# Kernel optimization log

Hardware: AMD Instinct MI355X
Metric: run time of the kernel (lower is better)

## Reference

```python
import jax, jax.numpy as jnp
import numpy as np


def _leaky(x):
    return jax.nn.leaky_relu(x, 0.01)


def _seq_query(sess_embed, query, batch_idx, B, W1, b1, W2, b2, a, ab):
    # attention weight per node, then segment-sum per session (vectorized torch.split loop)
    q = query[batch_idx]                                   # [T,D]
    w = jax.nn.sigmoid(q @ W1 + b1 + sess_embed @ W2 + b2) @ a + ab  # [T,1]
    return jax.ops.segment_sum(w * sess_embed, batch_idx, num_segments=B)


def setup_inputs() -> dict:
    key = jax.random.key(0)
    ks = jax.random.split(key, 24)
    N, D, B, L, E, G = 50000, 64, 512, 64, 1650000, 2
    T = B * L
    s = 1.0 / float(np.sqrt(D))
    rn = lambda k, sh: jax.random.normal(k, sh, dtype=jnp.float32) * s
    inp = {
        'sess_idx': jax.random.randint(ks[0], (T,), 0, N),
        'edges': jax.random.randint(ks[1], (2, T), 0, T),
        'batch_idx': jnp.repeat(jnp.arange(B, dtype=jnp.int32), L),
        'tar_poi': jax.random.randint(ks[2], (B,), 0, N),
        'y': (jax.random.uniform(ks[3], (B,)) > 0.5).astype(jnp.float32),
        'edge_index': jax.random.randint(ks[4], (2, E), 0, N),
        'dist_vec': jax.random.uniform(ks[5], (E,), dtype=jnp.float32),
        'poi_embed': rn(ks[6], (N, D)),
        'geo_W0': rn(ks[7], (G, D, D)),
        'geo_W1': rn(ks[8], (G, D, D)),
        'ggc_W': rn(ks[9], (D, D)),
        'gru_wih': rn(ks[10], (3 * D, D)),
        'gru_whh': rn(ks[11], (3 * D, D)),
        'gru_bih': jnp.zeros((3 * D,), jnp.float32),
        'gru_bhh': jnp.zeros((3 * D,), jnp.float32),
        'geoq_W1': rn(ks[12], (D, D)), 'geoq_b1': jnp.zeros((D,), jnp.float32),
        'geoq_W2': rn(ks[13], (D, D)), 'geoq_b2': jnp.zeros((D,), jnp.float32),
        'geoq_a': rn(ks[14], (D, 1)), 'geoq_ab': jnp.zeros((1,), jnp.float32),
        'sessq_W1': rn(ks[15], (D, D)), 'sessq_b1': jnp.zeros((D,), jnp.float32),
        'sessq_W2': rn(ks[16], (D, D)), 'sessq_b2': jnp.zeros((D,), jnp.float32),
        'sessq_a': rn(ks[17], (D, 1)), 'sessq_ab': jnp.zeros((1,), jnp.float32),
        'geo_proj': rn(ks[18], (D, D)),
        'sess_proj': rn(ks[19], (D, D)),
        'mlp_W1': rn(ks[20], (4 * D, D)), 'mlp_b1': jnp.zeros((D,), jnp.float32),
        'mlp_W2': rn(ks[21], (D, 1)), 'mlp_b2': jnp.zeros((1,), jnp.float32),
    }
    return inp


def reference(sess_idx, edges, batch_idx, tar_poi, y, edge_index, dist_vec,
              poi_embed, geo_W0, geo_W1, ggc_W, gru_wih, gru_whh, gru_bih, gru_bhh,
              geoq_W1, geoq_b1, geoq_W2, geoq_b2, geoq_a, geoq_ab,
              sessq_W1, sessq_b1, sessq_W2, sessq_b2, sessq_a, sessq_ab,
              geo_proj, sess_proj, mlp_W1, mlp_b1, mlp_W2, mlp_b2):
    N, D = poi_embed.shape
    B = tar_poi.shape[0]
    T = sess_idx.shape[0]
    row, col = edge_index[0], edge_index[1]

    # symmetric degree norm as in Geo_GCN (degree of col)
    deg = jax.ops.segment_sum(jnp.ones_like(dist_vec), col, num_segments=N)
    dinv = jnp.where(deg > 0, deg ** -0.5, 0.0)
    norm = dinv[row] * dinv[col]
    # NOTE: original applies exp(-d**2) twice (once in CTR.forward, once in Geo_GCN)
    dw = jnp.exp(-jnp.exp(-dist_vec ** 2) ** 2)
    val = (dw * norm)[:, None]                              # [E,1]

    geo_feat = poi_embed
    for i in range(geo_W0.shape[0]):
        side = jax.ops.segment_sum(val * geo_feat[col], row, num_segments=N)  # sparse mm
        geo_feat = _leaky(side @ geo_W0[i] + (geo_feat * side) @ geo_W1[i])
        geo_feat = geo_feat / jnp.maximum(
            jnp.linalg.norm(geo_feat, axis=-1, keepdims=True), 1e-12)

    geo_enc = _seq_query(geo_feat[sess_idx], geo_feat[tar_poi], batch_idx, B,
                         geoq_W1, geoq_b1, geoq_W2, geoq_b2, geoq_a, geoq_ab)
    geo_enc_p = geo_enc @ geo_proj

    # Neigh_pooling: mean aggregation at target node
    neigh = jax.ops.segment_sum(poi_embed[row], col, num_segments=N) \
        / jnp.maximum(deg, 1.0)[:, None]
    counts = jax.ops.segment_sum(jnp.ones((T,), poi_embed.dtype), batch_idx,
                                 num_segments=B)[:, None]
    geo_pool = (jax.ops.segment_sum(neigh[sess_idx], batch_idx, num_segments=B)
                / counts) @ geo_proj

    # GatedGraphConv, num_layers=1: sum-aggregate (h W), then GRU cell
    h = poi_embed[sess_idx]
    m = jax.ops.segment_sum((h @ ggc_W)[edges[0]], edges[1], num_segments=T)
    gi = m @ gru_wih.T + gru_bih
    gh = h @ gru_whh.T + gru_bhh
    ir, iz, i_n = jnp.split(gi, 3, axis=-1)
    hr, hz, h_n = jnp.split(gh, 3, axis=-1)
    r = jax.nn.sigmoid(ir + hr)
    z = jax.nn.sigmoid(iz + hz)
    n = jnp.tanh(i_n + r * h_n)
    sess_hidden = _leaky((1.0 - z) * n + z * h)

    sess_enc = _seq_query(sess_hidden, poi_embed[tar_poi], batch_idx, B,
                          sessq_W1, sessq_b1, sessq_W2, sessq_b2, sessq_a, sessq_ab)
    sess_enc_p = sess_enc @ sess_proj
    sess_pool = (jax.ops.segment_sum(poi_embed[sess_idx], batch_idx,
                                     num_segments=B) / counts) @ sess_proj

    bpr = lambda x, pos, neg: jax.nn.softplus((x * neg).sum(-1) - (x * pos).sum(-1))
    con_loss = bpr(geo_enc, geo_pool, sess_pool) + bpr(sess_enc, sess_pool, geo_pool)

    tar_embed = poi_embed[tar_poi]
    tar_geo_embed = geo_feat[tar_poi]
    feats = jnp.concatenate([tar_embed, tar_geo_embed, sess_enc_p, geo_enc_p], axis=-1)
    logits = (_leaky(feats @ mlp_W1 + mlp_b1) @ mlp_W2 + mlp_b2)[:, 0]
    return logits, con_loss, y, tar_embed, tar_geo_embed, geo_enc_p, sess_enc_p
```

## Files before the change

### kernel.cpp

```cpp
#include <hip/hip_runtime.h>
#include <math.h>

#define CDIV(a,b) (((a)+(b)-1)/(b))

__device__ __forceinline__ float wred(float v){
  #pragma unroll
  for (int o = 32; o; o >>= 1) v += __shfl_xor(v, o, 64);
  return v;
}
__device__ __forceinline__ float leakyf(float x){ return x > 0.f ? x : 0.01f * x; }
__device__ __forceinline__ float sigmf(float x){ return 1.f / (1.f + expf(-x)); }
__device__ __forceinline__ float softplusf(float x){
  return fmaxf(x, 0.f) + log1pf(expf(-fabsf(x)));
}

__global__ void k_deg2(const int* __restrict__ row, const int* __restrict__ col,
                       int* __restrict__ deg_row, int* __restrict__ deg_col,
                       int* __restrict__ rank_r, int* __restrict__ rank_c, int E){
  int e = blockIdx.x * blockDim.x + threadIdx.x;
  if (e < E){
    rank_r[e] = atomicAdd(&deg_row[row[e]], 1);
    rank_c[e] = atomicAdd(&deg_col[col[e]], 1);
  }
}

__global__ __launch_bounds__(1024) void k_scan2(const int* __restrict__ in0, int* __restrict__ out0,
                        const int* __restrict__ in1, int* __restrict__ out1,
                        float* __restrict__ dinv, int n){
  __shared__ int wincl[16];
  const int* in  = blockIdx.x ? in1 : in0;
  int* out       = blockIdx.x ? out1 : out0;
  int tid = threadIdx.x, lane = tid & 63, wv = tid >> 6;
  int carry = 0;
  for (int base = 0; base < n; base += 1024){
    int i = base + tid;
    int x = (i < n) ? in[i] : 0;
    int v = x;
    #pragma unroll
    for (int ofs = 1; ofs < 64; ofs <<= 1){
      int t = __shfl_up(v, ofs, 64);
      if (lane >= ofs) v += t;
    }
    if (lane == 63) wincl[wv] = v;
    __syncthreads();
    if (wv == 0 && lane < 16){
      int s = wincl[lane];
      #pragma unroll
      for (int ofs = 1; ofs < 16; ofs <<= 1){
        int t = __shfl_up(s, ofs, 64);
        if (lane >= ofs) s += t;
      }
      wincl[lane] = s;
    }
    __syncthreads();
    int woff = wv ? wincl[wv - 1] : 0;
    if (i < n) out[i] = carry + woff + v - x;
    carry += wincl[15];
    __syncthreads();
  }
  if (tid == 0) out[n] = carry;
  if (blockIdx.x == 1){
    for (int i = tid; i < n; i += 1024){
      int d = in1[i];
      dinv[i] = d > 0 ? 1.f / sqrtf((float)d) : 0.f;
    }
  }
}

__global__ __launch_bounds__(1024) void k_scanT(const int* __restrict__ in,
                                                int* __restrict__ out, int n){
  __shared__ int wincl[16];
  int tid = threadIdx.x, lane = tid & 63, wv = tid >> 6;
  int carry = 0;
  for (int base = 0; base < n; base += 1024){
    int i = base + tid;
    int x = (i < n) ? in[i] : 0;
    int v = x;
    #pragma unroll
    for (int ofs = 1; ofs < 64; ofs <<= 1){
      int t = __shfl_up(v, ofs, 64);
      if (lane >= ofs) v += t;
    }
    if (lane == 63) wincl[wv] = v;
    __syncthreads();
    if (wv == 0 && lane < 16){
      int s = wincl[lane];
      #pragma unroll
      for (int ofs = 1; ofs < 16; ofs <<= 1){
        int t = __shfl_up(s, ofs, 64);
        if (lane >= ofs) s += t;
      }
      wincl[lane] = s;
    }
    __syncthreads();
    int woff = wv ? wincl[wv - 1] : 0;
    if (i < n) out[i] = carry + woff + v - x;
    carry += wincl[15];
    __syncthreads();
  }
  if (tid == 0) out[n] = carry;
}

__global__ void k_degT(const int* __restrict__ e1, int* __restrict__ degt,
                       int* __restrict__ rankt, int T){
  int e = blockIdx.x * blockDim.x + threadIdx.x;
  if (e < T) rankt[e] = atomicAdd(&degt[e1[e]], 1);
}

__global__ void k_fillT(const int* __restrict__ e0, const int* __restrict__ e1,
                        const int* __restrict__ offs, const int* __restrict__ rankt,
                        int* __restrict__ csr_src, int T){
  int e = blockIdx.x * blockDim.x + threadIdx.x;
  if (e < T) csr_src[offs[e1[e]] + rankt[e]] = e0[e];
}

__global__ void k_fill2(const int* __restrict__ row, const int* __restrict__ col,
                        const float* __restrict__ dist, const float* __restrict__ dinv,
                        const int* __restrict__ offs_r, const int* __restrict__ rank_r,
                        int2* __restrict__ csr_cv,
                        const int* __restrict__ offs_c, const int* __restrict__ rank_c,
                        int* __restrict__ csr_row, int E){
  int e = blockIdx.x * blockDim.x + threadIdx.x;
  if (e < E){
    int r = row[e], c = col[e];
    int pr = offs_r[r] + rank_r[e];
    float d = dist[e];
    float t = expf(-d * d);
    float dw = expf(-t * t);
    csr_cv[pr] = make_int2(c, __float_as_int(dw * dinv[r] * dinv[c]));
    int pc = offs_c[c] + rank_c[e];
    csr_row[pc] = r;
  }
}

__global__ __launch_bounds__(512) void k_gcn2(const int* __restrict__ offs,
                      const int2* __restrict__ csr_cv,
                      const float* __restrict__ gfeat,
                      const float* __restrict__ W0, const float* __restrict__ W1,
                      float* __restrict__ out, int N){
  __shared__ float lw0[4096], lw1[4096];
  for (int i = threadIdx.x; i < 4096; i += 512){ lw0[i] = W0[i]; lw1[i] = W1[i]; }
  __syncthreads();
  int lane = threadIdx.x & 63, wave = threadIdx.x >> 6;
  int grp = lane >> 4, pos = lane & 15;
  const float4* gf4 = (const float4*)gfeat;
  int wgl = blockIdx.x * 8 + wave;
  int nw = gridDim.x * 8;
  for (int r = wgl; r < N; r += nw){
    int j0 = offs[r], j1 = offs[r + 1];
    float4 s4 = {0.f, 0.f, 0.f, 0.f};
    for (int jb = j0; jb < j1; jb += 64){
      int rem = j1 - jb;
      int cnt = rem < 64 ? rem : 64;
      int jj = jb + lane;
      int2 cv = make_int2(0, 0);
      if (jj < j1) cv = csr_cv[jj];
      int myc = cv.x; float myv = __int_as_float(cv.y);
      int rounds = (cnt + 3) >> 2;
      int kk = 0;
      for (; kk + 4 <= rounds; kk += 4){
        int e0 = (kk+0)*4 + grp, e1 = (kk+1)*4 + grp,
            e2 = (kk+2)*4 + grp, e3 = (kk+3)*4 + grp;
        int   c0 = __shfl(myc, e0, 64), c1 = __shfl(myc, e1, 64),
              c2 = __shfl(myc, e2, 64), c3 = __shfl(myc, e3, 64);
        float v0 = __shfl(myv, e0, 64), v1 = __shfl(myv, e1, 64),
              v2 = __shfl(myv, e2, 64), v3 = __shfl(myv, e3, 64);
        float4 f0 = gf4[(long)c0 * 16 + pos];
        float4 f1 = gf4[(long)c1 * 16 + pos];
        float4 f2 = gf4[(long)c2 * 16 + pos];
        float4 f3 = gf4[(long)c3 * 16 + pos];
        s4.x += v0*f0.x; s4.y += v0*f0.y; s4.z += v0*f0.z; s4.w += v0*f0.w;
        s4.x += v1*f1.x; s4.y += v1*f1.y; s4.z += v1*f1.z; s4.w += v1*f1.w;
        s4.x += v2*f2.x; s4.y += v2*f2.y; s4.z += v2*f2.z; s4.w += v2*f2.w;
        s4.x += v3*f3.x; s4.y += v3*f3.y; s4.z += v3*f3.z; s4.w += v3*f3.w;
      }
      for (; kk < rounds; kk++){
        int e = kk*4 + grp;
        int c = __shfl(myc, e, 64);
        float v = __shfl(myv, e, 64);
        float4 f = gf4[(long)c * 16 + pos];
        s4.x += v*f.x; s4.y += v*f.y; s4.z += v*f.z; s4.w += v*f.w;
      }
    }
    #pragma unroll
    for (int m = 16; m <= 32; m <<= 1){
      s4.x += __shfl_xor(s4.x, m, 64);
      s4.y += __shfl_xor(s4.y, m, 64);
      s4.z += __shfl_xor(s4.z, m, 64);
      s4.w += __shfl_xor(s4.w, m, 64);
    }
    int src = lane >> 2, cc = lane & 3;
    float sx = __shfl(s4.x, src, 64);
    float sy = __shfl(s4.y, src, 64);
    float sz = __shfl(s4.z, src, 64);
    float sw = __shfl(s4.w, src, 64);
    float s = (cc == 0) ? sx : (cc == 1) ? sy : (cc == 2) ? sz : sw;

    float g = gfeat[(long)r * 64 + lane];
    float acc = 0.f;
    #pragma unroll
    for (int k = 0; k < 64; k++){
      float sk = __shfl(s, k, 64);
      float gk = __shfl(g, k, 64);
      acc += sk * lw0[k * 64 + lane] + gk * sk * lw1[k * 64 + lane];
    }
    float x = leakyf(acc);
    float nrm = sqrtf(wred(x * x));
    out[(long)r * 64 + lane] = x / fmaxf(nrm, 1e-12f);
  }
}

__global__ __launch_bounds__(256) void k_pool_gather(const int* __restrict__ offs,
                      const int* __restrict__ csr_row,
                      const float* __restrict__ poi, float* __restrict__ neigh, int N){
  int lane = threadIdx.x & 63, wave = threadIdx.x >> 6;
  int grp = lane >> 4, pos = lane & 15;
  const float4* poi4 = (const float4*)poi;
  int wgl = blockIdx.x * 4 + wave;
  int nw = gridDim.x * 4;
  for (int n = wgl; n < N; n += nw){
    int j0 = offs[n], j1 = offs[n + 1];
    float4 s4 = {0.f, 0.f, 0.f, 0.f};
    for (int jb = j0; jb < j1; jb += 64){
      int rem = j1 - jb;
      int cnt = rem < 64 ? rem : 64;
      int jj = jb + lane;
      int myc = 0; float myw = 0.f;
      if (jj < j1){ myc = csr_row[jj]; myw = 1.f; }
      int rounds = (cnt + 3) >> 2;
      int kk = 0;
      for (; kk + 4 <= rounds; kk += 4){
        int e0 = (kk+0)*4 + grp, e1 = (kk+1)*4 + grp,
            e2 = (kk+2)*4 + grp, e3 = (kk+3)*4 + grp;
        int   c0 = __shfl(myc, e0, 64), c1 = __shfl(myc, e1, 64),
              c2 = __shfl(myc, e2, 64), c3 = __shfl(myc, e3, 64);
        float v0 = __shfl(myw, e0, 64), v1 = __shfl(myw, e1, 64),
              v2 = __shfl(myw, e2, 64), v3 = __shfl(myw, e3, 64);
        float4 f0 = poi4[(long)c0 * 16 + pos];
        float4 f1 = poi4[(long)c1 * 16 + pos];
        float4 f2 = poi4[(long)c2 * 16 + pos];
        float4 f3 = poi4[(long)c3 * 16 + pos];
        s4.x += v0*f0.x; s4.y += v0*f0.y; s4.z += v0*f0.z; s4.w += v0*f0.w;
        s4.x += v1*f1.x; s4.y += v1*f1.y; s4.z += v1*f1.z; s4.w += v1*f1.w;
        s4.x += v2*f2.x; s4.y += v2*f2.y; s4.z += v2*f2.z; s4.w += v2*f2.w;
        s4.x += v3*f3.x; s4.y += v3*f3.y; s4.z += v3*f3.z; s4.w += v3*f3.w;
      }
      for (; kk < rounds; kk++){
        int e = kk*4 + grp;
        int c = __shfl(myc, e, 64);
        float v = __shfl(myw, e, 64);
        float4 f = poi4[(long)c * 16 + pos];
        s4.x += v*f.x; s4.y += v*f.y; s4.z += v*f.z; s4.w += v*f.w;
      }
    }
    #pragma unroll
    for (int m = 16; m <= 32; m <<= 1){
      s4.x += __shfl_xor(s4.x, m, 64);
      s4.y += __shfl_xor(s4.y, m, 64);
      s4.z += __shfl_xor(s4.z, m, 64);
      s4.w += __shfl_xor(s4.w, m, 64);
    }
    int src = lane >> 2, cc = lane & 3;
    float sx = __shfl(s4.x, src, 64);
    float sy = __shfl(s4.y, src, 64);
    float sz = __shfl(s4.z, src, 64);
    float sw = __shfl(s4.w, src, 64);
    float s = (cc == 0) ? sx : (cc == 1) ? sy : (cc == 2) ? sz : sw;
    float inv = 1.f / fmaxf((float)(j1 - j0), 1.f);
    neigh[(long)n * 64 + lane] = s * inv;
  }
}

template<bool GATHER>
__global__ __launch_bounds__(256) void k_gemm64(const float* __restrict__ X, const int* __restrict__ ridx,
                         const float* __restrict__ W, const float* __restrict__ bias,
                         float* __restrict__ Y, int M){
  __shared__ float lw[4096];
  for (int i = threadIdx.x; i < 4096; i += 256) lw[i] = W[i];
  __syncthreads();
  int lane = threadIdx.x & 63, wave = threadIdx.x >> 6;
  int wgl = blockIdx.x * 4 + wave;
  int nw = gridDim.x * 4;
  for (int r = wgl; r < M; r += nw){
    long src = GATHER ? (long)ridx[r] : (long)r;
    float x = X[src * 64 + lane];
    float acc = bias ? bias[lane] : 0.f;
    #pragma unroll
    for (int k = 0; k < 64; k++) acc += __shfl(x, k, 64) * lw[k * 64 + lane];
    Y[(long)r * 64 + lane] = acc;
  }
}

template<bool GATHER_S>
__global__ __launch_bounds__(256) void k_seqq(const float* __restrict__ sbase, const int* __restrict__ sidx,
                       const float* __restrict__ qbase, const int* __restrict__ tar,
                       const float* __restrict__ W1, const float* __restrict__ b1,
                       const float* __restrict__ W2, const float* __restrict__ b2,
                       const float* __restrict__ a, const float* __restrict__ ab,
                       const float* __restrict__ proj,
                       float* __restrict__ enc_out, float* __restrict__ proj_out, int L){
  __shared__ float lw1[4096], lw2[4096], la[64], lb[64];
  __shared__ float red[4][64];
  __shared__ float encs[64];
  int tid = threadIdx.x;
  for (int i = tid; i < 4096; i += 256){ lw1[i] = W1[i]; lw2[i] = W2[i]; }
  if (tid < 64){ la[tid] = a[tid]; lb[tid] = b1[tid] + b2[tid]; }
  __syncthreads();
  int lane = tid & 63, wave = tid >> 6;
  int b = blockIdx.x;
  float q = qbase[(long)tar[b] * 64 + lane];
  float ab0 = ab[0];
  float hq = lb[lane];
  #pragma unroll
  for (int k = 0; k < 64; k++) hq += __shfl(q, k, 64) * lw1[k * 64 + lane];
  float acc = 0.f;
  for (int tl = wave; tl < L; tl += 4){
    int t = b * L + tl;
    long srow = GATHER_S ? (long)sidx[t] : (long)t;
    float s = sbase[srow * 64 + lane];
    float h = hq;
    #pragma unroll
    for (int k = 0; k < 64; k++) h += __shfl(s, k, 64) * lw2[k * 64 + lane];
    float sg = sigmf(h);
    float w = wred(sg * la[lane]) + ab0;
    acc += w * s;
  }
  red[wave][lane] = acc;
  __syncthreads();
  if (tid < 64){
    float e = red[0][tid] + red[1][tid] + red[2][tid] + red[3][tid];
    encs[tid] = e;
    enc_out[(long)b * 64 + tid] = e;
  }
  __syncthreads();
  for (int i = tid; i < 4096; i += 256) lw1[i] = proj[i];
  __syncthreads();
  if (tid < 64){
    float ap = 0.f;
    #pragma unroll
    for (int k = 0; k < 64; k++) ap += encs[k] * lw1[k * 64 + tid];
    proj_out[(long)b * 64 + tid] = ap;
  }
}

__global__ __launch_bounds__(256) void k_pool(const float* __restrict__ neigh, const float* __restrict__ poi,
                       const int* __restrict__ sidx,
                       const float* __restrict__ projG, const float* __restrict__ projS,
                       float* __restrict__ gpool, float* __restrict__ spool, int L){
  __shared__ float lwg[4096], lws[4096];
  __shared__ float r1[4][64], r2[4][64];
  __shared__ float p1s[64], p2s[64];
  int tid = threadIdx.x, lane = tid & 63, wave = tid >> 6, b = blockIdx.x;
  for (int i = tid; i < 4096; i += 256){ lwg[i] = projG[i]; lws[i] = projS[i]; }
  float a1 = 0.f, a2 = 0.f;
  for (int tl = wave; tl < L; tl += 4){
    long idx = sidx[b * L + tl];
    a1 += neigh[idx * 64 + lane];
    a2 += poi[idx * 64 + lane];
  }
  r1[wave][lane] = a1; r2[wave][lane] = a2;
  __syncthreads();
  if (tid < 64){
    float inv = 1.f / (float)L;
    p1s[tid] = (r1[0][tid] + r1[1][tid] + r1[2][tid] + r1[3][tid]) * inv;
    p2s[tid] = (r2[0][tid] + r2[1][tid] + r2[2][tid] + r2[3][tid]) * inv;
  }
  __syncthreads();
  if (tid < 64){
    float ag = 0.f, as = 0.f;
    #pragma unroll
    for (int k = 0; k < 64; k++){
      ag += p1s[k] * lwg[k * 64 + tid];
      as += p2s[k] * lws[k * 64 + tid];
    }
    gpool[(long)b * 64 + tid] = ag;
    spool[(long)b * 64 + tid] = as;
  }
}

__global__ __launch_bounds__(256) void k_gi(const float* __restrict__ hw,
                     const int* __restrict__ offs_t, const int* __restrict__ csr_src,
                     const float* __restrict__ wih, const float* __restrict__ bih,
                     float* __restrict__ gi, int T){
  __shared__ float lw[64 * 193];
  __shared__ float lb[192];
  int tid = threadIdx.x, lane = tid & 63, wave = tid >> 6;
  if (tid < 192) lb[tid] = bih[tid];
  for (int idx = tid; idx < 192 * 64; idx += 256){
    int j = idx >> 6, k = idx & 63;
    lw[k * 193 + j] = wih[idx];
  }
  __syncthreads();
  int r0 = blockIdx.x * 4 + wave, nw = gridDim.x * 4;
  for (int t = r0; t < T; t += nw){
    int j0 = offs_t[t], j1 = offs_t[t + 1];
    float x = 0.f;
    for (int j = j0; j < j1; j++)
      x += hw[(long)csr_src[j] * 64 + lane];
    float a0 = lb[lane], a1 = lb[64 + lane], a2 = lb[128 + lane];
    #pragma unroll
    for (int k = 0; k < 64; k++){
      float xk = __shfl(x, k, 64);
      a0 += xk * lw[k * 193 + lane];
      a1 += xk * lw[k * 193 + 64 + lane];
      a2 += xk * lw[k * 193 + 128 + lane];
    }
    gi[(long)t * 192 + lane] = a0;
    gi[(long)t * 192 + 64 + lane] = a1;
    gi[(long)t * 192 + 128 + lane] = a2;
  }
}

__global__ __launch_bounds__(256) void k_gru2(const float* __restrict__ gi,
                       const float* __restrict__ poi, const int* __restrict__ sidx,
                       const float* __restrict__ whh, const float* __restrict__ bhh,
                       float* __restrict__ out, int T){
  __shared__ float lw[64 * 193];
  __shared__ float lb[192];
  int tid = threadIdx.x, lane = tid & 63, wave = tid >> 6;
  if (tid < 192) lb[tid] = bhh[tid];
  for (int idx = tid; idx < 192 * 64; idx += 256){
    int j = idx >> 6, k = idx & 63;
    lw[k * 193 + j] = whh[idx];
  }
  __syncthreads();
  int r0 = blockIdx.x * 4 + wave, nw = gridDim.x * 4;
  for (int t = r0; t < T; t += nw){
    float h = poi[(long)sidx[t] * 64 + lane];
    float b0 = lb[lane], b1 = lb[64 + lane], b2 = lb[128 + lane];
    #pragma unroll
    for (int k = 0; k < 64; k++){
      float hk = __shfl(h, k, 64);
      b0 += hk * lw[k * 193 + lane];
      b1 += hk * lw[k * 193 + 64 + lane];
      b2 += hk * lw[k * 193 + 128 + lane];
    }
    float r = sigmf(gi[(long)t * 192 + lane] + b0);
    float z = sigmf(gi[(long)t * 192 + 64 + lane] + b1);
    float n = tanhf(gi[(long)t * 192 + 128 + lane] + r * b2);
    float nh = (1.f - z) * n + z * h;
    out[(long)t * 64 + lane] = leakyf(nh);
  }
}

__global__ __launch_bounds__(64) void k_final(
    const float* __restrict__ poi, const float* __restrict__ gf,
    const int* __restrict__ tar,
    const float* __restrict__ geo_enc, const float* __restrict__ sess_enc,
    const float* __restrict__ gpool, const float* __restrict__ spool,
    const float* __restrict__ mW1, const float* __restrict__ mb1,
    const float* __restrict__ mW2, const float* __restrict__ mb2,
    const float* __restrict__ y, float* __restrict__ out, int B){
  int b = blockIdx.x, c = threadIdx.x;
  long tp = tar[b];
  long offT = 3L * B, offG = 3L * B + (long)B * 64;
  long offGP = 3L * B + 2L * B * 64, offSP = 3L * B + 3L * B * 64;
  float f0 = poi[tp * 64 + c];
  float f1 = gf[tp * 64 + c];
  float f2 = out[offSP + (long)b * 64 + c];
  float f3 = out[offGP + (long)b * 64 + c];
  float ge = geo_enc[(long)b * 64 + c], se = sess_enc[(long)b * 64 + c];
  float gp = gpool[(long)b * 64 + c], sp = spool[(long)b * 64 + c];
  float d1 = wred(ge * sp);
  float d2 = wred(ge * gp);
  float d3 = wred(se * gp);
  float d4 = wred(se * sp);
  float con = softplusf(d1 - d2) + softplusf(d3 - d4);
  float acc = mb1[c];
  #pragma unroll
  for (int k = 0; k < 64; k++){
    acc += __shfl(f0, k, 64) * mW1[k * 64 + c];
    acc += __shfl(f1, k, 64) * mW1[(64 + k) * 64 + c];
    acc += __shfl(f2, k, 64) * mW1[(128 + k) * 64 + c];
    acc += __shfl(f3, k, 64) * mW1[(192 + k) * 64 + c];
  }
  float hid = leakyf(acc);
  float lsum = wred(hid * mW2[c]);
  if (c == 0){
    out[b] = lsum + mb2[0];
    out[B + b] = con;
    out[2L * B + b] = y[b];
  }
  out[offT + (long)b * 64 + c] = f0;
  out[offG + (long)b * 64 + c] = f1;
}

extern "C" void kernel_launch(void* const* d_in, const int* in_sizes, int n_in,
                              void* d_out, int out_size, void* d_ws, size_t ws_size,
                              hipStream_t stream){
  const int*   sess_idx = (const int*)d_in[0];
  const int*   edges    = (const int*)d_in[1];
  const int*   tar_poi  = (const int*)d_in[3];
  const float* y        = (const float*)d_in[4];
  const int*   eidx     = (const int*)d_in[5];
  const float* dist     = (const float*)d_in[6];
  const float* poi      = (const float*)d_in[7];
  const float* geoW0    = (const float*)d_in[8];
  const float* geoW1    = (const float*)d_in[9];
  const float* ggcW     = (const float*)d_in[10];
  const float* wih      = (const float*)d_in[11];
  const float* whh      = (const float*)d_in[12];
  const float* bih      = (const float*)d_in[13];
  const float* bhh      = (const float*)d_in[14];
  const float* geoqW1   = (const float*)d_in[15];
  const float* geoqb1   = (const float*)d_in[16];
  const float* geoqW2   = (const float*)d_in[17];
  const float* geoqb2   = (const float*)d_in[18];
  const float* geoqa    = (const float*)d_in[19];
  const float* geoqab   = (const float*)d_in[20];
  const float* sessqW1  = (const float*)d_in[21];
  const float* sessqb1  = (const float*)d_in[22];
  const float* sessqW2  = (const float*)d_in[23];
  const float* sessqb2  = (const float*)d_in[24];
  const float* sessqa   = (const float*)d_in[25];
  const float* sessqab  = (const float*)d_in[26];
  const float* geo_proj = (const float*)d_in[27];
  const float* sess_proj= (const float*)d_in[28];
  const float* mW1      = (const float*)d_in[29];
  const float* mb1      = (const float*)d_in[30];
  const float* mW2      = (const float*)d_in[31];
  const float* mb2      = (const float*)d_in[32];

  const int T = in_sizes[0];
  const int B = in_sizes[3];
  const int E = in_sizes[5] / 2;
  const int N = in_sizes[7] / 64;
  const int G = in_sizes[8] / 4096;
  const int L = T / B;
  const int* erow = eidx;
  const int* ecol = eidx + E;
  const int* e0 = edges;
  const int* e1 = edges + T;

  char* w = (char*)d_ws;
  size_t off = 0;
  auto nxt = [&](size_t bytes)->void*{
    void* p = w + off; off = (off + bytes + 255) & ~(size_t)255; return p;
  };
  int*   deg_row = (int*)  nxt((size_t)N * 4);
  int*   deg_col = (int*)  nxt((size_t)N * 4);
  int*   offs_r  = (int*)  nxt((size_t)(N + 1) * 4);
  int*   offs_c  = (int*)  nxt((size_t)(N + 1) * 4);
  float* dinv    = (float*)nxt((size_t)N * 4);
  int*   degt    = (int*)  nxt((size_t)T * 4);
  int*   rankt   = (int*)  nxt((size_t)T * 4);
  int*   offs_t  = (int*)  nxt((size_t)(T + 1) * 4);
  int*   csr_src = (int*)  nxt((size_t)T * 4);
  float* gf1     = (float*)nxt((size_t)N * 256);
  float* geo_enc = (float*)nxt((size_t)B * 256);
  float* sess_enc= (float*)nxt((size_t)B * 256);
  float* gpool   = (float*)nxt((size_t)B * 256);
  float* spool   = (float*)nxt((size_t)B * 256);
  float* gf0     = (float*)nxt((size_t)N * 256);
  int2*  csr_cv  = (int2*) nxt((size_t)E * 8);
  int*   csr_row = (int*)  nxt((size_t)E * 4);
  float* poolbuf = (float*)nxt((size_t)N * 256);
  float* hw      = (float*)nxt((size_t)T * 256);
  float* gi      = gf0;
  float* neigh   = poolbuf;
  float* sessh   = hw;
  int*   rank_r  = (int*)poolbuf;
  int*   rank_c  = rank_r + E;
  float* outf    = (float*)d_out;

  const long offGP = 3L * B + 2L * B * 64;
  const long offSP = 3L * B + 3L * B * 64;

  hipMemsetAsync(deg_row, 0, (size_t)N * 4, stream);
  hipMemsetAsync(deg_col, 0, (size_t)N * 4, stream);
  k_deg2<<<CDIV(E,256),256,0,stream>>>(erow, ecol, deg_row, deg_col, rank_r, rank_c, E);
  k_scan2<<<2,1024,0,stream>>>(deg_row, offs_r, deg_col, offs_c, dinv, N);
  k_fill2<<<CDIV(E,256),256,0,stream>>>(erow, ecol, dist, dinv,
                                        offs_r, rank_r, csr_cv,
                                        offs_c, rank_c, csr_row, E);

  const float* cur = poi;
  float* nextb = (G & 1) ? gf1 : gf0;
  for (int g = 0; g < G; g++){
    k_gcn2<<<1024,512,0,stream>>>(offs_r, csr_cv, cur,
                                  geoW0 + (size_t)g * 4096, geoW1 + (size_t)g * 4096,
                                  nextb, N);
    cur = nextb;
    nextb = (nextb == gf0) ? gf1 : gf0;
  }
  const float* gf = cur;

  k_seqq<true><<<B,256,0,stream>>>(gf, sess_idx, gf, tar_poi,
                                   geoqW1, geoqb1, geoqW2, geoqb2, geoqa, geoqab,
                                   geo_proj, geo_enc, outf + offGP, L);

  k_pool_gather<<<2048,256,0,stream>>>(offs_c, csr_row, poi, neigh, N);
  k_pool<<<B,256,0,stream>>>(neigh, poi, sess_idx, geo_proj, sess_proj,
                             gpool, spool, L);

  k_gemm64<true><<<2048,256,0,stream>>>(poi, sess_idx, ggcW, nullptr, hw, T);
  hipMemsetAsync(degt, 0, (size_t)T * 4, stream);
  k_degT<<<CDIV(T,256),256,0,stream>>>(e1, degt, rankt, T);
  k_scanT<<<1,1024,0,stream>>>(degt, offs_t, T);
  k_fillT<<<CDIV(T,256),256,0,stream>>>(e0, e1, offs_t, rankt, csr_src, T);
  k_gi<<<1024,256,0,stream>>>(hw, offs_t, csr_src, wih, bih, gi, T);
  k_gru2<<<1024,256,0,stream>>>(gi, poi, sess_idx, whh, bhh, sessh, T);

  k_seqq<false><<<B,256,0,stream>>>(sessh, nullptr, poi, tar_poi,
                                    sessqW1, sessqb1, sessqW2, sessqb2, sessqa, sessqab,
                                    sess_proj, sess_enc, outf + offSP, L);

  k_final<<<B,64,0,stream>>>(poi, gf, tar_poi, geo_enc, sess_enc, gpool, spool,
                             mW1, mb1, mW2, mb2, y, outf, B);
}
```

Measured before the change: 853.6 us.

## Split GCN layer into gather and matmul kernels; unroll gather by eight

The fused GCN kernel, which needed 32KB of LDS for weights and was launched with 512 threads, is split into two kernels. The first is a gather-only SpMM kernel with no shared memory, which should allow higher occupancy and more loads in flight. The second is a separate dense-transform kernel that reads the aggregated rows from a scratch buffer. Both gather loops are unrolled from 4 to 8 independent float4 loads, and the final per-row write becomes a float4 store from one lane group. The split adds an extra global write and read of an N×64 intermediate per layer, plus one more launch.

```diff
diff --git a/kernel.cpp b/kernel.cpp
--- a/kernel.cpp
+++ b/kernel.cpp
@@ -133,19 +133,15 @@
   }
 }
 
-__global__ __launch_bounds__(512) void k_gcn2(const int* __restrict__ offs,
+__global__ __launch_bounds__(256) void k_gather(const int* __restrict__ offs,
                       const int2* __restrict__ csr_cv,
                       const float* __restrict__ gfeat,
-                      const float* __restrict__ W0, const float* __restrict__ W1,
-                      float* __restrict__ out, int N){
-  __shared__ float lw0[4096], lw1[4096];
-  for (int i = threadIdx.x; i < 4096; i += 512){ lw0[i] = W0[i]; lw1[i] = W1[i]; }
-  __syncthreads();
+                      float* __restrict__ side, int N){
   int lane = threadIdx.x & 63, wave = threadIdx.x >> 6;
   int grp = lane >> 4, pos = lane & 15;
   const float4* gf4 = (const float4*)gfeat;
-  int wgl = blockIdx.x * 8 + wave;
-  int nw = gridDim.x * 8;
+  int wgl = blockIdx.x * 4 + wave;
+  int nw = gridDim.x * 4;
   for (int r = wgl; r < N; r += nw){
     int j0 = offs[r], j1 = offs[r + 1];
     float4 s4 = {0.f, 0.f, 0.f, 0.f};
@@ -158,21 +154,21 @@
       int myc = cv.x; float myv = __int_as_float(cv.y);
       int rounds = (cnt + 3) >> 2;
       int kk = 0;
-      for (; kk + 4 <= rounds; kk += 4){
-        int e0 = (kk+0)*4 + grp, e1 = (kk+1)*4 + grp,
-            e2 = (kk+2)*4 + grp, e3 = (kk+3)*4 + grp;
-        int   c0 = __shfl(myc, e0, 64), c1 = __shfl(myc, e1, 64),
-              c2 = __shfl(myc, e2, 64), c3 = __shfl(myc, e3, 64);
-        float v0 = __shfl(myv, e0, 64), v1 = __shfl(myv, e1, 64),
-              v2 = __shfl(myv, e2, 64), v3 = __shfl(myv, e3, 64);
-        float4 f0 = gf4[(long)c0 * 16 + pos];
-        float4 f1 = gf4[(long)c1 * 16 + pos];
-        float4 f2 = gf4[(long)c2 * 16 + pos];
-        float4 f3 = gf4[(long)c3 * 16 + pos];
-        s4.x += v0*f0.x; s4.y += v0*f0.y; s4.z += v0*f0.z; s4.w += v0*f0.w;
-        s4.x += v1*f1.x; s4.y += v1*f1.y; s4.z += v1*f1.z; s4.w += v1*f1.w;
-        s4.x += v2*f2.x; s4.y += v2*f2.y; s4.z += v2*f2.z; s4.w += v2*f2.w;
-        s4.x += v3*f3.x; s4.y += v3*f3.y; s4.z += v3*f3.z; s4.w += v3*f3.w;
+      for (; kk + 8 <= rounds; kk += 8){
+        int c[8]; float v[8]; float4 f[8];
+        #pragma unroll
+        for (int u = 0; u < 8; u++){
+          int e = (kk + u) * 4 + grp;
+          c[u] = __shfl(myc, e, 64);
+          v[u] = __shfl(myv, e, 64);
+        }
+        #pragma unroll
+        for (int u = 0; u < 8; u++) f[u] = gf4[(long)c[u] * 16 + pos];
+        #pragma unroll
+        for (int u = 0; u < 8; u++){
+          s4.x += v[u]*f[u].x; s4.y += v[u]*f[u].y;
+          s4.z += v[u]*f[u].z; s4.w += v[u]*f[u].w;
+        }
       }
       for (; kk < rounds; kk++){
         int e = kk*4 + grp;
@@ -189,13 +185,22 @@
       s4.z += __shfl_xor(s4.z, m, 64);
       s4.w += __shfl_xor(s4.w, m, 64);
     }
-    int src = lane >> 2, cc = lane & 3;
-    float sx = __shfl(s4.x, src, 64);
-    float sy = __shfl(s4.y, src, 64);
-    float sz = __shfl(s4.z, src, 64);
-    float sw = __shfl(s4.w, src, 64);
-    float s = (cc == 0) ? sx : (cc == 1) ? sy : (cc == 2) ? sz : sw;
-
+    if (grp == 0) ((float4*)side)[(long)r * 16 + pos] = s4;
+  }
+}
+
+__global__ __launch_bounds__(256) void k_gcnmm(const float* __restrict__ side,
+                      const float* __restrict__ gfeat,
+                      const float* __restrict__ W0, const float* __restrict__ W1,
+                      float* __restrict__ out, int N){
+  __shared__ float lw0[4096], lw1[4096];
+  for (int i = threadIdx.x; i < 4096; i += 256){ lw0[i] = W0[i]; lw1[i] = W1[i]; }
+  __syncthreads();
+  int lane = threadIdx.x & 63, wave = threadIdx.x >> 6;
+  int wgl = blockIdx.x * 4 + wave;
+  int nw = gridDim.x * 4;
+  for (int r = wgl; r < N; r += nw){
+    float s = side[(long)r * 64 + lane];
     float g = gfeat[(long)r * 64 + lane];
     float acc = 0.f;
     #pragma unroll
@@ -229,21 +234,21 @@
       if (jj < j1){ myc = csr_row[jj]; myw = 1.f; }
       int rounds = (cnt + 3) >> 2;
       int kk = 0;
-      for (; kk + 4 <= rounds; kk += 4){
-        int e0 = (kk+0)*4 + grp, e1 = (kk+1)*4 + grp,
-            e2 = (kk+2)*4 + grp, e3 = (kk+3)*4 + grp;
-        int   c0 = __shfl(myc, e0, 64), c1 = __shfl(myc, e1, 64),
-              c2 = __shfl(myc, e2, 64), c3 = __shfl(myc, e3, 64);
-        float v0 = __shfl(myw, e0, 64), v1 = __shfl(myw, e1, 64),
-              v2 = __shfl(myw, e2, 64), v3 = __shfl(myw, e3, 64);
-        float4 f0 = poi4[(long)c0 * 16 + pos];
-        float4 f1 = poi4[(long)c1 * 16 + pos];
-        float4 f2 = poi4[(long)c2 * 16 + pos];
-        float4 f3 = poi4[(long)c3 * 16 + pos];
-        s4.x += v0*f0.x; s4.y += v0*f0.y; s4.z += v0*f0.z; s4.w += v0*f0.w;
-        s4.x += v1*f1.x; s4.y += v1*f1.y; s4.z += v1*f1.z; s4.w += v1*f1.w;
-        s4.x += v2*f2.x; s4.y += v2*f2.y; s4.z += v2*f2.z; s4.w += v2*f2.w;
-        s4.x += v3*f3.x; s4.y += v3*f3.y; s4.z += v3*f3.z; s4.w += v3*f3.w;
+      for (; kk + 8 <= rounds; kk += 8){
+        int c[8]; float v[8]; float4 f[8];
+        #pragma unroll
+        for (int u = 0; u < 8; u++){
+          int e = (kk + u) * 4 + grp;
+          c[u] = __shfl(myc, e, 64);
+          v[u] = __shfl(myw, e, 64);
+        }
+        #pragma unroll
+        for (int u = 0; u < 8; u++) f[u] = poi4[(long)c[u] * 16 + pos];
+        #pragma unroll
+        for (int u = 0; u < 8; u++){
+          s4.x += v[u]*f[u].x; s4.y += v[u]*f[u].y;
+          s4.z += v[u]*f[u].z; s4.w += v[u]*f[u].w;
+        }
       }
       for (; kk < rounds; kk++){
         int e = kk*4 + grp;
@@ -260,14 +265,11 @@
       s4.z += __shfl_xor(s4.z, m, 64);
       s4.w += __shfl_xor(s4.w, m, 64);
     }
-    int src = lane >> 2, cc = lane & 3;
-    float sx = __shfl(s4.x, src, 64);
-    float sy = __shfl(s4.y, src, 64);
-    float sz = __shfl(s4.z, src, 64);
-    float sw = __shfl(s4.w, src, 64);
-    float s = (cc == 0) ? sx : (cc == 1) ? sy : (cc == 2) ? sz : sw;
-    float inv = 1.f / fmaxf((float)(j1 - j0), 1.f);
-    neigh[(long)n * 64 + lane] = s * inv;
+    if (grp == 0){
+      float inv = 1.f / fmaxf((float)(j1 - j0), 1.f);
+      float4 o = make_float4(s4.x * inv, s4.y * inv, s4.z * inv, s4.w * inv);
+      ((float4*)neigh)[(long)n * 16 + pos] = o;
+    }
   }
 }
 
@@ -557,6 +559,7 @@
   float* poolbuf = (float*)nxt((size_t)N * 256);
   float* hw      = (float*)nxt((size_t)T * 256);
   float* gi      = gf0;
+  float* side    = poolbuf;
   float* neigh   = poolbuf;
   float* sessh   = hw;
   int*   rank_r  = (int*)poolbuf;
@@ -577,9 +580,9 @@
   const float* cur = poi;
   float* nextb = (G & 1) ? gf1 : gf0;
   for (int g = 0; g < G; g++){
-    k_gcn2<<<1024,512,0,stream>>>(offs_r, csr_cv, cur,
-                                  geoW0 + (size_t)g * 4096, geoW1 + (size_t)g * 4096,
-                                  nextb, N);
+    k_gather<<<2048,256,0,stream>>>(offs_r, csr_cv, cur, side, N);
+    k_gcnmm<<<2048,256,0,stream>>>(side, cur, geoW0 + (size_t)g * 4096,
+                                   geoW1 + (size_t)g * 4096, nextb, N);
     cur = nextb;
     nextb = (nextb == gf0) ? gf1 : gf0;
   }
```

New measurement: 894.7 us. 4.8% more time.
